# Kernel optimization log

Measured on AMD Instinct MI355X. Metric: run time of the kernel, lower is better.

The kernel has to match this reference:

```python
import jax, jax.numpy as jnp
import numpy as np

B, S, D, K = 64, 512, 512, 1024
DECAY = 0.99
EPS = 1e-05
COMMITMENT_COST = 0.25
PAD_IDX = 0


def setup_inputs() -> dict:
    key = jax.random.key(0)
    k1, k2, k3 = jax.random.split(key, 3)
    inputs = jax.random.normal(k1, (B, S, D), dtype=jnp.float32)
    padding_mask = jax.random.bernoulli(k2, 0.1, (B, S))
    codebook_w = jax.random.normal(k3, (K, D), dtype=jnp.float32) * 0.02
    codebook_w = codebook_w.at[PAD_IDX].set(0.0)  # padding_idx row zeroed
    ema_cluster_size = jnp.zeros((K,), dtype=jnp.float32)
    ema_w = codebook_w  # _ema_w initialized as copy of codebook
    return {"inputs": inputs, "padding_mask": padding_mask,
            "codebook_w": codebook_w, "ema_cluster_size": ema_cluster_size,
            "ema_w": ema_w}


def reference(inputs, padding_mask, codebook_w, ema_cluster_size, ema_w):
    input_shape = inputs.shape
    flat = inputs.reshape(-1, D)                      # [N, D]
    mask = padding_mask.reshape(-1)                   # [N], True = pad

    # squared euclidean distances: [N, K]
    dist = (jnp.sum(flat * flat, axis=1, keepdims=True)
            + jnp.sum(codebook_w * codebook_w, axis=1)
            - 2.0 * flat @ codebook_w.T)
    # non-padded tokens cannot pick code 0; padded tokens must pick code 0
    inf = jnp.float32(np.inf)
    col0 = jnp.where(mask, dist[:, 0], inf)
    rest = jnp.where(mask[:, None], inf, dist[:, 1:])
    dist = jnp.concatenate([col0[:, None], rest], axis=1)

    idx = jnp.argmin(dist, axis=1)                    # [N] int
    quantized = codebook_w[idx].reshape(input_shape)  # gather == onehot @ W

    num_nonpad = jnp.sum(~mask).astype(jnp.float32) * D
    e_latent_loss = jnp.sum((jax.lax.stop_gradient(quantized) - inputs) ** 2) / num_nonpad
    loss = COMMITMENT_COST * e_latent_loss

    # EMA codebook update (training branch, discard_ema_cluster_sizes=False)
    counts = jax.ops.segment_sum(jnp.ones_like(idx, dtype=jnp.float32), idx,
                                 num_segments=K)      # sum(encodings, 0)
    dw = jax.ops.segment_sum(flat, idx, num_segments=K)  # encodings.T @ flat
    cs = ema_cluster_size * DECAY + (1.0 - DECAY) * counts
    n = jnp.sum(cs)
    cs = (cs + EPS) / (n + K * EPS) * n
    new_ema_w = ema_w * DECAY + (1.0 - DECAY) * dw
    new_codebook = new_ema_w / cs[:, None]
    new_codebook = new_codebook.at[PAD_IDX].set(0.0)

    # straight-through estimator
    quantized_st = inputs + jax.lax.stop_gradient(quantized - inputs)

    avg_probs = counts / counts.shape[0] / (flat.shape[0] / K) if False else counts / flat.shape[0]
    perplexity = jnp.exp(-jnp.sum(avg_probs * jnp.log(avg_probs + 1e-10)))

    return (quantized_st, idx.reshape(input_shape[:-1]), loss, perplexity,
            cs, new_ema_w, new_codebook)
```

## Files before the change

### kernel.cpp

```cpp
#include <hip/hip_runtime.h>
#include <math.h>

#define N_TOK 32768
#define DDIM  512
#define KCODE 1024
#define DECAYF 0.99f
#define EPSV 1e-5f
#define CCOST 0.25f
#define MARGIN 1e-3f

typedef float f32x4 __attribute__((ext_vector_type(4)));
typedef short short8v __attribute__((ext_vector_type(8)));

__device__ __forceinline__ unsigned short f2bf(float f) {
  unsigned u = __float_as_uint(f);
  u += 0x7fffu + ((u >> 16) & 1u);
  return (unsigned short)(u >> 16);
}
__device__ __forceinline__ float bf2f(unsigned short h) {
  return __uint_as_float(((unsigned)h) << 16);
}

__device__ __forceinline__ unsigned ordf(float f) {
  unsigned u = __float_as_uint(f);
  return (u & 0x80000000u) ? ~u : (u | 0x80000000u);
}
__device__ __forceinline__ float ord2f(unsigned v) {
  unsigned u = (v & 0x80000000u) ? (v & 0x7fffffffu) : ~v;
  return __uint_as_float(u);
}
__device__ __forceinline__ void top2m(unsigned long long& a1, unsigned long long& a2,
                                      unsigned long long b1, unsigned long long b2) {
  unsigned long long m1 = a1 < b1 ? a1 : b1;
  unsigned long long hi = a1 < b1 ? b1 : a1;
  unsigned long long m2 = a2 < b2 ? a2 : b2;
  a2 = m2 < hi ? m2 : hi;
  a1 = m1;
}

__device__ __forceinline__ void stage16(const void* g, char* lds_base, int lane) {
#if __has_builtin(__builtin_amdgcn_global_load_lds)
  __builtin_amdgcn_global_load_lds((const __attribute__((address_space(1))) void*)g,
                                   (__attribute__((address_space(3))) void*)lds_base,
                                   16, 0, 0);
#else
  *(float4*)(lds_base + lane * 16) = *(const float4*)g;
#endif
}

__global__ __launch_bounds__(256) void convert_fused(
    const float* __restrict__ x, const float* __restrict__ w,
    unsigned short* __restrict__ xhi, unsigned short* __restrict__ xlo,
    unsigned short* __restrict__ whi, unsigned short* __restrict__ wlo,
    float* __restrict__ wn)
{
  int b = blockIdx.x;
  int tid = threadIdx.x;
  if (b < 16384) {
    size_t i = (size_t)b * 256 + tid;
    float4 v = *(const float4*)(x + i * 4);
    ushort4 h, l;
    h.x = f2bf(v.x); l.x = f2bf(v.x - bf2f(h.x));
    h.y = f2bf(v.y); l.y = f2bf(v.y - bf2f(h.y));
    h.z = f2bf(v.z); l.z = f2bf(v.z - bf2f(h.z));
    h.w = f2bf(v.w); l.w = f2bf(v.w - bf2f(h.w));
    *(ushort4*)(xhi + i * 4) = h;
    *(ushort4*)(xlo + i * 4) = l;
  } else {
    int k = (b - 16384) * 4 + (tid >> 6);
    int lane = tid & 63;
    double s = 0.0;
    #pragma unroll
    for (int it = 0; it < 2; it++) {
      size_t off = (size_t)k * DDIM + (lane + 64 * it) * 4;
      float4 v = *(const float4*)(w + off);
      s += (double)v.x*(double)v.x + (double)v.y*(double)v.y
         + (double)v.z*(double)v.z + (double)v.w*(double)v.w;
      ushort4 h, l;
      h.x = f2bf(v.x); l.x = f2bf(v.x - bf2f(h.x));
      h.y = f2bf(v.y); l.y = f2bf(v.y - bf2f(h.y));
      h.z = f2bf(v.z); l.z = f2bf(v.z - bf2f(h.z));
      h.w = f2bf(v.w); l.w = f2bf(v.w - bf2f(h.w));
      *(ushort4*)(whi + off) = h;
      *(ushort4*)(wlo + off) = l;
    }
    for (int o = 32; o > 0; o >>= 1) s += __shfl_down(s, o, 64);
    if (lane == 0) wn[k] = (float)s;
  }
}

__global__ __launch_bounds__(256) void dist_mfma(
    const unsigned short* __restrict__ xhi, const unsigned short* __restrict__ xlo,
    const unsigned short* __restrict__ whi, const unsigned short* __restrict__ wlo,
    const float* __restrict__ wn,
    unsigned long long* __restrict__ k1buf, unsigned long long* __restrict__ k2buf)
{
  __shared__ __align__(16) short sAh[128 * 32];
  __shared__ __align__(16) short sAl[128 * 32];
  __shared__ __align__(16) short sBh[128 * 32];
  __shared__ __align__(16) short sBl[128 * 32];
  const int tid = threadIdx.x;
  const int wv = tid >> 6, lane = tid & 63;
  const int wg = (blockIdx.x & 7) * 256 + (blockIdx.x >> 3);
  const int tb = wg >> 3, kb = wg & 7;
  const int row0 = tb * 128, col0 = kb * 128;
  const int rw = wv & 1, cw = wv >> 1;
  const int q = lane >> 4, cl = lane & 15;
  const int swz = (cl >> 1) & 3;

  f32x4 acc[4][4];
  #pragma unroll
  for (int mt = 0; mt < 4; mt++)
    #pragma unroll
    for (int nt = 0; nt < 4; nt++) acc[mt][nt] = (f32x4){0.f, 0.f, 0.f, 0.f};

  const int cA0 = wv * 64 + lane;
  const int r0 = cA0 >> 2;
  const int s0 = (cA0 & 3) ^ ((r0 >> 1) & 3);
  const size_t aoff0 = (size_t)(row0 + r0) * 1024 + (size_t)s0 * 16;
  const size_t boff0 = (size_t)(col0 + r0) * 1024 + (size_t)s0 * 16;
  const char* pxh = (const char*)xhi;
  const char* pxl = (const char*)xlo;
  const char* pwh = (const char*)whi;
  const char* pwl = (const char*)wlo;

  const int aidx = (rw * 64 + cl) * 32 + (q ^ swz) * 8;
  const int bidx = (cw * 64 + cl) * 32 + (q ^ swz) * 8;

  for (int ks = 0; ks < 16; ks++) {
    const int k2 = ks * 64;
    __syncthreads();
    stage16(pxh + aoff0 + k2,         (char*)sAh + wv * 1024, lane);
    stage16(pxh + aoff0 + 65536 + k2, (char*)sAh + (wv + 4) * 1024, lane);
    stage16(pxl + aoff0 + k2,         (char*)sAl + wv * 1024, lane);
    stage16(pxl + aoff0 + 65536 + k2, (char*)sAl + (wv + 4) * 1024, lane);
    stage16(pwh + boff0 + k2,         (char*)sBh + wv * 1024, lane);
    stage16(pwh + boff0 + 65536 + k2, (char*)sBh + (wv + 4) * 1024, lane);
    stage16(pwl + boff0 + k2,         (char*)sBl + wv * 1024, lane);
    stage16(pwl + boff0 + 65536 + k2, (char*)sBl + (wv + 4) * 1024, lane);
    __syncthreads();

    short8v ah[4], bh[4];
    #pragma unroll
    for (int mt = 0; mt < 4; mt++) ah[mt] = *(const short8v*)(sAh + aidx + mt * 512);
    #pragma unroll
    for (int nt = 0; nt < 4; nt++) bh[nt] = *(const short8v*)(sBh + bidx + nt * 512);
    #pragma unroll
    for (int mt = 0; mt < 4; mt++)
      #pragma unroll
      for (int nt = 0; nt < 4; nt++)
        acc[mt][nt] = __builtin_amdgcn_mfma_f32_16x16x32_bf16(ah[mt], bh[nt], acc[mt][nt], 0, 0, 0);

    short8v bl[4];
    #pragma unroll
    for (int nt = 0; nt < 4; nt++) bl[nt] = *(const short8v*)(sBl + bidx + nt * 512);
    #pragma unroll
    for (int mt = 0; mt < 4; mt++)
      #pragma unroll
      for (int nt = 0; nt < 4; nt++)
        acc[mt][nt] = __builtin_amdgcn_mfma_f32_16x16x32_bf16(ah[mt], bl[nt], acc[mt][nt], 0, 0, 0);

    short8v al[4];
    #pragma unroll
    for (int mt = 0; mt < 4; mt++) al[mt] = *(const short8v*)(sAl + aidx + mt * 512);
    #pragma unroll
    for (int mt = 0; mt < 4; mt++)
      #pragma unroll
      for (int nt = 0; nt < 4; nt++)
        acc[mt][nt] = __builtin_amdgcn_mfma_f32_16x16x32_bf16(al[mt], bh[nt], acc[mt][nt], 0, 0, 0);
  }

  float wnv[4];
  #pragma unroll
  for (int nt = 0; nt < 4; nt++) wnv[nt] = wn[col0 + cw * 64 + nt * 16 + cl];

  const int strip = kb * 2 + cw;
  #pragma unroll
  for (int mt = 0; mt < 4; mt++) {
    #pragma unroll
    for (int r = 0; r < 4; r++) {
      unsigned long long k1 = ~0ull, k2 = ~0ull;
      #pragma unroll
      for (int nt = 0; nt < 4; nt++) {
        int kk = col0 + cw * 64 + nt * 16 + cl;
        float dist = fmaf(-2.f, acc[mt][nt][r], wnv[nt]);
        unsigned long long key = (kk == 0) ? ~0ull
            : ((unsigned long long)ordf(dist) << 32) | (unsigned)kk;
        if (key < k1) { k2 = k1; k1 = key; }
        else if (key < k2) k2 = key;
      }
      #pragma unroll
      for (int off = 8; off > 0; off >>= 1) {
        unsigned long long o1 = __shfl_down(k1, off, 16);
        unsigned long long o2 = __shfl_down(k2, off, 16);
        top2m(k1, k2, o1, o2);
      }
      if (cl == 0) {
        int rowg = row0 + rw * 64 + mt * 16 + q * 4 + r;
        k1buf[strip * N_TOK + rowg] = k1;
        k2buf[strip * N_TOK + rowg] = k2;
      }
    }
  }
}

__global__ __launch_bounds__(1024) void combine_kernel(
    const unsigned long long* __restrict__ k1buf, const unsigned long long* __restrict__ k2buf,
    const int* __restrict__ mask,
    int* __restrict__ idx_i, int* __restrict__ flagList, int* __restrict__ flagcnt,
    int* __restrict__ counts_i)
{
  __shared__ int lh[KCODE];
  int tid = threadIdx.x;
  lh[tid] = 0;
  __syncthreads();
  int t = blockIdx.x * 1024 + tid;
  unsigned long long a1 = ~0ull, a2 = ~0ull;
  #pragma unroll
  for (int s = 0; s < 16; s++)
    top2m(a1, a2, k1buf[s * N_TOK + t], k2buf[s * N_TOK + t]);
  int bi = (int)(a1 & 0xffffffffu);
  float d1 = ord2f((unsigned)(a1 >> 32));
  float d2 = ord2f((unsigned)(a2 >> 32));
  int pad = mask[t];
  int id = pad ? 0 : bi;
  idx_i[t] = id;
  atomicAdd(&lh[id], 1);
  if (!pad && (d2 - d1) < MARGIN) {
    int p = atomicAdd(flagcnt, 1);
    flagList[p] = t;
  }
  __syncthreads();
  if (lh[tid] > 0) atomicAdd(&counts_i[tid], lh[tid]);
}

__global__ __launch_bounds__(256) void refine_kernel(
    const float* __restrict__ x, const float* __restrict__ w,
    const float* __restrict__ wn32,
    const int* __restrict__ flagList, const int* __restrict__ flagcnt,
    int* __restrict__ idx_i, int* __restrict__ counts_i)
{
  __shared__ double xd[DDIM];
  __shared__ double redbuf[4];
  __shared__ float A32sh;
  __shared__ float bv_s[256];
  __shared__ int   bi_s[256];
  int tid = threadIdx.x;
  int lane = tid & 63, wid = tid >> 6;
  int nf = *flagcnt;
  for (int fi = blockIdx.x; fi < nf; fi += gridDim.x) {
    int token = flagList[fi];
    double part = 0.0;
    for (int e = tid; e < DDIM; e += 256) {
      double v = (double)x[(size_t)token * DDIM + e];
      xd[e] = v;
      part += v * v;
    }
    for (int o = 32; o > 0; o >>= 1) part += __shfl_down(part, o, 64);
    if (lane == 0) redbuf[wid] = part;
    __syncthreads();
    if (tid == 0) {
      double a64 = redbuf[0] + redbuf[1] + redbuf[2] + redbuf[3];
      A32sh = (float)a64;
    }
    __syncthreads();
    float A32 = A32sh;
    float bv = 3.4e38f; int bi = 0x7fffffff;
    for (int k = tid; k < KCODE; k += 256) {
      if (k == 0) continue;
      const float4* wr = (const float4*)(w + (size_t)k * DDIM);
      double dot = 0.0;
      #pragma unroll 4
      for (int dq = 0; dq < DDIM / 4; dq++) {
        float4 wv = wr[dq];
        dot += xd[dq*4+0]*(double)wv.x + xd[dq*4+1]*(double)wv.y
             + xd[dq*4+2]*(double)wv.z + xd[dq*4+3]*(double)wv.w;
      }
      float M = (float)dot;
      float AB = A32 + wn32[k];
      float dist = AB - 2.0f * M;
      if (dist < bv) { bv = dist; bi = k; }
    }
    bv_s[tid] = bv; bi_s[tid] = bi;
    __syncthreads();
    for (int st = 128; st > 0; st >>= 1) {
      if (tid < st) {
        if (bv_s[tid+st] < bv_s[tid] ||
            (bv_s[tid+st] == bv_s[tid] && bi_s[tid+st] < bi_s[tid])) {
          bv_s[tid] = bv_s[tid+st]; bi_s[tid] = bi_s[tid+st];
        }
      }
      __syncthreads();
    }
    if (tid == 0) {
      int old = idx_i[token];
      int nw = bi_s[0];
      if (nw != old) {
        idx_i[token] = nw;
        atomicSub(&counts_i[old], 1);
        atomicAdd(&counts_i[nw], 1);
      }
    }
    __syncthreads();
  }
}

__global__ __launch_bounds__(1024) void scan_kernel(
    const int* __restrict__ counts_i, int* __restrict__ offsets, int* __restrict__ cursor)
{
  __shared__ int tmp[1024];
  int t = threadIdx.x;
  int c = counts_i[t];
  tmp[t] = c;
  __syncthreads();
  for (int off = 1; off < 1024; off <<= 1) {
    int v = (t >= off) ? tmp[t - off] : 0;
    __syncthreads();
    tmp[t] += v;
    __syncthreads();
  }
  int ex = tmp[t] - c;
  offsets[t] = ex;
  cursor[t] = ex;
}

__global__ __launch_bounds__(1024) void scatter_kernel(
    const int* __restrict__ idx_i, int* __restrict__ cursor, int* __restrict__ bucket)
{
  __shared__ int lh[KCODE];
  __shared__ int lb[KCODE];
  int tid = threadIdx.x;
  lh[tid] = 0;
  __syncthreads();
  int token = blockIdx.x * 1024 + tid;
  int id = idx_i[token];
  int r = atomicAdd(&lh[id], 1);
  __syncthreads();
  if (lh[tid] > 0) lb[tid] = atomicAdd(&cursor[tid], lh[tid]);
  __syncthreads();
  bucket[lb[id] + r] = token;
}

__global__ __launch_bounds__(256) void quant_kernel(
    const float* __restrict__ x, const float* __restrict__ w,
    const int* __restrict__ idx_i,
    float* __restrict__ out_q, float* __restrict__ out_idx, float* __restrict__ losssum)
{
  __shared__ float sred[4];
  int tid = threadIdx.x;
  int qd = tid & 127, h = tid >> 7;
  float s = 0.f;
  #pragma unroll
  for (int i = 0; i < 8; i++) {
    int token = blockIdx.x * 16 + i * 2 + h;
    int idx = idx_i[token];
    float4 xv = *(const float4*)(x + (size_t)token * DDIM + qd * 4);
    float4 wv = *(const float4*)(w + (size_t)idx * DDIM + qd * 4);
    *(float4*)(out_q + (size_t)token * DDIM + qd * 4) = wv;
    if (qd == 0) out_idx[token] = (float)idx;
    float dx = wv.x - xv.x, dy = wv.y - xv.y, dz = wv.z - xv.z, dww = wv.w - xv.w;
    s += dx*dx + dy*dy + dz*dz + dww*dww;
  }
  for (int o = 32; o > 0; o >>= 1) s += __shfl_down(s, o, 64);
  int lane = tid & 63, wid = tid >> 6;
  if (lane == 0) sred[wid] = s;
  __syncthreads();
  if (tid == 0) atomicAdd(losssum, sred[0] + sred[1] + sred[2] + sred[3]);
}

__global__ __launch_bounds__(128) void dw_kernel(
    const float* __restrict__ x, const int* __restrict__ bucket,
    const int* __restrict__ idx_i, float* __restrict__ dw)
{
  int b0 = blockIdx.x * 32;
  int t = threadIdx.x;
  int ent = bucket[b0 + (t & 31)];
  int eid = idx_i[ent];
  int tok0 = __shfl(ent, 0, 64);
  int cur  = __shfl(eid, 0, 64);
  float4 acc = make_float4(0.f, 0.f, 0.f, 0.f);
  float4 nv = *(const float4*)(x + (size_t)tok0 * DDIM + t * 4);
  for (int j = 0; j < 32; j++) {
    float4 v = nv;
    int id = __shfl(eid, j, 64);
    if (j < 31) {
      int tn = __shfl(ent, j + 1, 64);
      nv = *(const float4*)(x + (size_t)tn * DDIM + t * 4);
    }
    if (id != cur) {
      float* p = dw + (size_t)cur * DDIM + t * 4;
      atomicAdd(p + 0, acc.x); atomicAdd(p + 1, acc.y);
      atomicAdd(p + 2, acc.z); atomicAdd(p + 3, acc.w);
      acc = make_float4(0.f, 0.f, 0.f, 0.f);
      cur = id;
    }
    acc.x += v.x; acc.y += v.y; acc.z += v.z; acc.w += v.w;
  }
  float* p = dw + (size_t)cur * DDIM + t * 4;
  atomicAdd(p + 0, acc.x); atomicAdd(p + 1, acc.y);
  atomicAdd(p + 2, acc.z); atomicAdd(p + 3, acc.w);
}

__global__ __launch_bounds__(1024) void stats_kernel(
    const int* __restrict__ counts_i, const float* __restrict__ ema_cs,
    const float* __restrict__ losssum,
    float* __restrict__ out_loss, float* __restrict__ out_perp,
    float* __restrict__ out_cs)
{
  __shared__ float sbuf[17];
  int k = threadIdx.x;
  float cnt = (float)counts_i[k];
  float csr = ema_cs[k] * DECAYF + (1.f - DECAYF) * cnt;
  float v = csr;
  for (int o = 32; o > 0; o >>= 1) v += __shfl_down(v, o, 64);
  int lane = k & 63, wid = k >> 6;
  if (lane == 0) sbuf[wid] = v;
  __syncthreads();
  if (k == 0) { float n = 0.f; for (int i = 0; i < 16; i++) n += sbuf[i]; sbuf[16] = n; }
  __syncthreads();
  float n = sbuf[16];
  out_cs[k] = (csr + EPSV) / (n + (float)KCODE * EPSV) * n;
  __syncthreads();
  float p = cnt / (float)N_TOK;
  v = p * logf(p + 1e-10f);
  for (int o = 32; o > 0; o >>= 1) v += __shfl_down(v, o, 64);
  if (lane == 0) sbuf[wid] = v;
  __syncthreads();
  if (k == 0) {
    float s = 0.f; for (int i = 0; i < 16; i++) s += sbuf[i];
    out_perp[0] = expf(-s);
    float nonpad = (float)(N_TOK - counts_i[0]);
    out_loss[0] = CCOST * losssum[0] / (nonpad * (float)DDIM);
  }
}

__global__ __launch_bounds__(256) void ema_kernel(
    const float* __restrict__ ema_w, const float* __restrict__ dw,
    const float* __restrict__ cs,
    float* __restrict__ out_ema, float* __restrict__ out_cb)
{
  int i = blockIdx.x * 256 + threadIdx.x;
  int e = i * 4;
  int k = e >> 9;
  float4 dv = *(const float4*)(dw + e);
  float4 ew = *(const float4*)(ema_w + e);
  float4 ne;
  ne.x = ew.x * DECAYF + (1.f - DECAYF) * dv.x;
  ne.y = ew.y * DECAYF + (1.f - DECAYF) * dv.y;
  ne.z = ew.z * DECAYF + (1.f - DECAYF) * dv.z;
  ne.w = ew.w * DECAYF + (1.f - DECAYF) * dv.w;
  *(float4*)(out_ema + e) = ne;
  float4 cb;
  if (k == 0) { cb.x = 0.f; cb.y = 0.f; cb.z = 0.f; cb.w = 0.f; }
  else {
    float csk = cs[k];
    cb.x = ne.x / csk; cb.y = ne.y / csk; cb.z = ne.z / csk; cb.w = ne.w / csk;
  }
  *(float4*)(out_cb + e) = cb;
}

extern "C" void kernel_launch(void* const* d_in, const int* in_sizes, int n_in,
                              void* d_out, int out_size, void* d_ws, size_t ws_size,
                              hipStream_t stream) {
  const float* x      = (const float*)d_in[0];
  const int*   mask   = (const int*)d_in[1];
  const float* w      = (const float*)d_in[2];
  const float* ema_cs = (const float*)d_in[3];
  const float* ema_w  = (const float*)d_in[4];
  float* out = (float*)d_out;

  float* out_q    = out;
  float* out_idx  = out + 16777216;
  float* out_loss = out + 16809984;
  float* out_perp = out + 16809985;
  float* out_cs   = out + 16809986;
  float* out_ema  = out + 16811010;
  float* out_cb   = out + 17335298;

  unsigned short* xhi = (unsigned short*)out_q;
  unsigned short* xlo = xhi + (size_t)N_TOK * DDIM;

  char* ws = (char*)d_ws;
  int*   counts_i = (int*)  (ws + 0);
  float* dw       = (float*)(ws + 4096);
  float* losssum  = (float*)(ws + 2101248);
  int*   flagcnt  = (int*)  (ws + 2101252);
  int*   offsets  = (int*)  (ws + 2101312);
  int*   cursor   = (int*)  (ws + 2105408);
  float* wn       = (float*)(ws + 2109504);
  int*   idx_i    = (int*)  (ws + 2113600);
  int*   bucket   = (int*)  (ws + 2244672);
  unsigned short* whi = (unsigned short*)(ws + 2375744);
  unsigned short* wlo = (unsigned short*)(ws + 3424320);
  unsigned long long* k1buf = (unsigned long long*)(ws + 4472896);
  unsigned long long* k2buf = (unsigned long long*)(ws + 8667200);
  int*   flagList = (int*)  (ws + 12861504);

  hipMemsetAsync(ws, 0, 2101256, stream);
  convert_fused<<<16384 + 256, 256, 0, stream>>>(x, w, xhi, xlo, whi, wlo, wn);
  dist_mfma<<<(N_TOK / 128) * 8, 256, 0, stream>>>(xhi, xlo, whi, wlo, wn, k1buf, k2buf);
  combine_kernel<<<N_TOK / 1024, 1024, 0, stream>>>(k1buf, k2buf, mask, idx_i, flagList, flagcnt, counts_i);
  refine_kernel<<<1024, 256, 0, stream>>>(x, w, wn, flagList, flagcnt, idx_i, counts_i);
  scan_kernel<<<1, 1024, 0, stream>>>(counts_i, offsets, cursor);
  scatter_kernel<<<N_TOK / 1024, 1024, 0, stream>>>(idx_i, cursor, bucket);
  quant_kernel<<<N_TOK / 16, 256, 0, stream>>>(x, w, idx_i, out_q, out_idx, losssum);
  dw_kernel<<<N_TOK / 32, 128, 0, stream>>>(x, bucket, idx_i, dw);
  stats_kernel<<<1, 1024, 0, stream>>>(counts_i, ema_cs, losssum, out_loss, out_perp, out_cs);
  ema_kernel<<<KCODE * DDIM / 4 / 256, 256, 0, stream>>>(ema_w, dw, out_cs, out_ema, out_cb);
}
```

Before: 409.4 us.

## Double-buffer LDS tiles in distance GEMM and raise MFMA wave priority

The distance MFMA kernel now keeps two sets of LDS buffers, so global-to-LDS staging of the next K-slice is issued before the MFMAs on the current slice run. This removes one barrier per step and lets memory loads overlap with compute. s_setprio is also raised around the MFMA bursts to favour math issue. The cost is doubled LDS use (64KB per block), which may lower occupancy.

```diff
diff --git a/kernel.cpp b/kernel.cpp
--- a/kernel.cpp
+++ b/kernel.cpp
@@ -95,10 +95,14 @@
     const float* __restrict__ wn,
     unsigned long long* __restrict__ k1buf, unsigned long long* __restrict__ k2buf)
 {
-  __shared__ __align__(16) short sAh[128 * 32];
-  __shared__ __align__(16) short sAl[128 * 32];
-  __shared__ __align__(16) short sBh[128 * 32];
-  __shared__ __align__(16) short sBl[128 * 32];
+  __shared__ __align__(16) short sAh0[128 * 32];
+  __shared__ __align__(16) short sAl0[128 * 32];
+  __shared__ __align__(16) short sBh0[128 * 32];
+  __shared__ __align__(16) short sBl0[128 * 32];
+  __shared__ __align__(16) short sAh1[128 * 32];
+  __shared__ __align__(16) short sAl1[128 * 32];
+  __shared__ __align__(16) short sBh1[128 * 32];
+  __shared__ __align__(16) short sBl1[128 * 32];
   const int tid = threadIdx.x;
   const int wv = tid >> 6, lane = tid & 63;
   const int wg = (blockIdx.x & 7) * 256 + (blockIdx.x >> 3);
@@ -127,48 +131,67 @@
   const int aidx = (rw * 64 + cl) * 32 + (q ^ swz) * 8;
   const int bidx = (cw * 64 + cl) * 32 + (q ^ swz) * 8;
 
-  for (int ks = 0; ks < 16; ks++) {
-    const int k2 = ks * 64;
-    __syncthreads();
-    stage16(pxh + aoff0 + k2,         (char*)sAh + wv * 1024, lane);
-    stage16(pxh + aoff0 + 65536 + k2, (char*)sAh + (wv + 4) * 1024, lane);
-    stage16(pxl + aoff0 + k2,         (char*)sAl + wv * 1024, lane);
-    stage16(pxl + aoff0 + 65536 + k2, (char*)sAl + (wv + 4) * 1024, lane);
-    stage16(pwh + boff0 + k2,         (char*)sBh + wv * 1024, lane);
-    stage16(pwh + boff0 + 65536 + k2, (char*)sBh + (wv + 4) * 1024, lane);
-    stage16(pwl + boff0 + k2,         (char*)sBl + wv * 1024, lane);
-    stage16(pwl + boff0 + 65536 + k2, (char*)sBl + (wv + 4) * 1024, lane);
-    __syncthreads();
-
-    short8v ah[4], bh[4];
-    #pragma unroll
-    for (int mt = 0; mt < 4; mt++) ah[mt] = *(const short8v*)(sAh + aidx + mt * 512);
-    #pragma unroll
-    for (int nt = 0; nt < 4; nt++) bh[nt] = *(const short8v*)(sBh + bidx + nt * 512);
-    #pragma unroll
-    for (int mt = 0; mt < 4; mt++)
-      #pragma unroll
-      for (int nt = 0; nt < 4; nt++)
-        acc[mt][nt] = __builtin_amdgcn_mfma_f32_16x16x32_bf16(ah[mt], bh[nt], acc[mt][nt], 0, 0, 0);
-
-    short8v bl[4];
-    #pragma unroll
-    for (int nt = 0; nt < 4; nt++) bl[nt] = *(const short8v*)(sBl + bidx + nt * 512);
-    #pragma unroll
-    for (int mt = 0; mt < 4; mt++)
-      #pragma unroll
-      for (int nt = 0; nt < 4; nt++)
-        acc[mt][nt] = __builtin_amdgcn_mfma_f32_16x16x32_bf16(ah[mt], bl[nt], acc[mt][nt], 0, 0, 0);
-
-    short8v al[4];
-    #pragma unroll
-    for (int mt = 0; mt < 4; mt++) al[mt] = *(const short8v*)(sAl + aidx + mt * 512);
-    #pragma unroll
-    for (int mt = 0; mt < 4; mt++)
-      #pragma unroll
-      for (int nt = 0; nt < 4; nt++)
-        acc[mt][nt] = __builtin_amdgcn_mfma_f32_16x16x32_bf16(al[mt], bh[nt], acc[mt][nt], 0, 0, 0);
-  }
+#define STAGE_STEP(KS, AH, AL, BH, BL) do {                                   \
+    const int kk2_ = (KS) * 64;                                               \
+    stage16(pxh + aoff0 + kk2_,         (char*)(AH) + wv * 1024, lane);       \
+    stage16(pxh + aoff0 + 65536 + kk2_, (char*)(AH) + (wv + 4) * 1024, lane); \
+    stage16(pxl + aoff0 + kk2_,         (char*)(AL) + wv * 1024, lane);       \
+    stage16(pxl + aoff0 + 65536 + kk2_, (char*)(AL) + (wv + 4) * 1024, lane); \
+    stage16(pwh + boff0 + kk2_,         (char*)(BH) + wv * 1024, lane);       \
+    stage16(pwh + boff0 + 65536 + kk2_, (char*)(BH) + (wv + 4) * 1024, lane); \
+    stage16(pwl + boff0 + kk2_,         (char*)(BL) + wv * 1024, lane);       \
+    stage16(pwl + boff0 + 65536 + kk2_, (char*)(BL) + (wv + 4) * 1024, lane); \
+  } while (0)
+
+#define COMPUTE_STEP(AH, AL, BH, BL) do {                                     \
+    short8v ah_[4], bh_[4];                                                   \
+    _Pragma("unroll")                                                         \
+    for (int mt = 0; mt < 4; mt++) ah_[mt] = *(const short8v*)((AH) + aidx + mt * 512); \
+    _Pragma("unroll")                                                         \
+    for (int nt = 0; nt < 4; nt++) bh_[nt] = *(const short8v*)((BH) + bidx + nt * 512); \
+    __builtin_amdgcn_s_setprio(1);                                            \
+    _Pragma("unroll")                                                         \
+    for (int mt = 0; mt < 4; mt++)                                            \
+      _Pragma("unroll")                                                       \
+      for (int nt = 0; nt < 4; nt++)                                          \
+        acc[mt][nt] = __builtin_amdgcn_mfma_f32_16x16x32_bf16(ah_[mt], bh_[nt], acc[mt][nt], 0, 0, 0); \
+    __builtin_amdgcn_s_setprio(0);                                            \
+    short8v bl_[4];                                                           \
+    _Pragma("unroll")                                                         \
+    for (int nt = 0; nt < 4; nt++) bl_[nt] = *(const short8v*)((BL) + bidx + nt * 512); \
+    __builtin_amdgcn_s_setprio(1);                                            \
+    _Pragma("unroll")                                                         \
+    for (int mt = 0; mt < 4; mt++)                                            \
+      _Pragma("unroll")                                                       \
+      for (int nt = 0; nt < 4; nt++)                                          \
+        acc[mt][nt] = __builtin_amdgcn_mfma_f32_16x16x32_bf16(ah_[mt], bl_[nt], acc[mt][nt], 0, 0, 0); \
+    __builtin_amdgcn_s_setprio(0);                                            \
+    short8v al_[4];                                                           \
+    _Pragma("unroll")                                                         \
+    for (int mt = 0; mt < 4; mt++) al_[mt] = *(const short8v*)((AL) + aidx + mt * 512); \
+    __builtin_amdgcn_s_setprio(1);                                            \
+    _Pragma("unroll")                                                         \
+    for (int mt = 0; mt < 4; mt++)                                            \
+      _Pragma("unroll")                                                       \
+      for (int nt = 0; nt < 4; nt++)                                          \
+        acc[mt][nt] = __builtin_amdgcn_mfma_f32_16x16x32_bf16(al_[mt], bh_[nt], acc[mt][nt], 0, 0, 0); \
+    __builtin_amdgcn_s_setprio(0);                                            \
+  } while (0)
+
+  STAGE_STEP(0, sAh0, sAl0, sBh0, sBl0);
+  __syncthreads();
+
+  #pragma unroll 1
+  for (int ks = 0; ks < 16; ks += 2) {
+    STAGE_STEP(ks + 1, sAh1, sAl1, sBh1, sBl1);
+    COMPUTE_STEP(sAh0, sAl0, sBh0, sBl0);
+    __syncthreads();
+    if (ks + 2 < 16) STAGE_STEP(ks + 2, sAh0, sAl0, sBh0, sBl0);
+    COMPUTE_STEP(sAh1, sAl1, sBh1, sBl1);
+    __syncthreads();
+  }
+#undef STAGE_STEP
+#undef COMPUTE_STEP
 
   float wnv[4];
   #pragma unroll
```

Result: no change. 403.1 us (-1.6%).

## Drop split-bf16 low parts; use single bf16 GEMM with wider refine margin

Applied to the files above, without the earlier changes.

Stops computing bf16 low-residual halves of inputs and codebook, and the distance GEMM now runs one bf16 MFMA pass per tile instead of three (hi*hi, hi*lo, lo*hi). This cuts conversion traffic, LDS staging and MFMA work to about a third. To make up for the lower precision, the top-2 ambiguity margin goes from 1e-3 to 0.05, so more tokens get flagged for exact fp32 refinement, and the refine kernel grid is doubled to handle them. The risk is a much larger refine workload and possible wrong argmin picks if the margin is too tight for plain bf16 error.

```diff
diff --git a/kernel.cpp b/kernel.cpp
--- a/kernel.cpp
+++ b/kernel.cpp
@@ -7,7 +7,7 @@
 #define DECAYF 0.99f
 #define EPSV 1e-5f
 #define CCOST 0.25f
-#define MARGIN 1e-3f
+#define MARGIN 0.05f
 
 typedef float f32x4 __attribute__((ext_vector_type(4)));
 typedef short short8v __attribute__((ext_vector_type(8)));
@@ -50,8 +50,7 @@
 
 __global__ __launch_bounds__(256) void convert_fused(
     const float* __restrict__ x, const float* __restrict__ w,
-    unsigned short* __restrict__ xhi, unsigned short* __restrict__ xlo,
-    unsigned short* __restrict__ whi, unsigned short* __restrict__ wlo,
+    unsigned short* __restrict__ xhi, unsigned short* __restrict__ whi,
     float* __restrict__ wn)
 {
   int b = blockIdx.x;
@@ -59,13 +58,12 @@
   if (b < 16384) {
     size_t i = (size_t)b * 256 + tid;
     float4 v = *(const float4*)(x + i * 4);
-    ushort4 h, l;
-    h.x = f2bf(v.x); l.x = f2bf(v.x - bf2f(h.x));
-    h.y = f2bf(v.y); l.y = f2bf(v.y - bf2f(h.y));
-    h.z = f2bf(v.z); l.z = f2bf(v.z - bf2f(h.z));
-    h.w = f2bf(v.w); l.w = f2bf(v.w - bf2f(h.w));
+    ushort4 h;
+    h.x = f2bf(v.x);
+    h.y = f2bf(v.y);
+    h.z = f2bf(v.z);
+    h.w = f2bf(v.w);
     *(ushort4*)(xhi + i * 4) = h;
-    *(ushort4*)(xlo + i * 4) = l;
   } else {
     int k = (b - 16384) * 4 + (tid >> 6);
     int lane = tid & 63;
@@ -76,13 +74,12 @@
       float4 v = *(const float4*)(w + off);
       s += (double)v.x*(double)v.x + (double)v.y*(double)v.y
          + (double)v.z*(double)v.z + (double)v.w*(double)v.w;
-      ushort4 h, l;
-      h.x = f2bf(v.x); l.x = f2bf(v.x - bf2f(h.x));
-      h.y = f2bf(v.y); l.y = f2bf(v.y - bf2f(h.y));
-      h.z = f2bf(v.z); l.z = f2bf(v.z - bf2f(h.z));
-      h.w = f2bf(v.w); l.w = f2bf(v.w - bf2f(h.w));
+      ushort4 h;
+      h.x = f2bf(v.x);
+      h.y = f2bf(v.y);
+      h.z = f2bf(v.z);
+      h.w = f2bf(v.w);
       *(ushort4*)(whi + off) = h;
-      *(ushort4*)(wlo + off) = l;
     }
     for (int o = 32; o > 0; o >>= 1) s += __shfl_down(s, o, 64);
     if (lane == 0) wn[k] = (float)s;
@@ -90,15 +87,12 @@
 }
 
 __global__ __launch_bounds__(256) void dist_mfma(
-    const unsigned short* __restrict__ xhi, const unsigned short* __restrict__ xlo,
-    const unsigned short* __restrict__ whi, const unsigned short* __restrict__ wlo,
+    const unsigned short* __restrict__ xhi, const unsigned short* __restrict__ whi,
     const float* __restrict__ wn,
     unsigned long long* __restrict__ k1buf, unsigned long long* __restrict__ k2buf)
 {
-  __shared__ __align__(16) short sAh[128 * 32];
-  __shared__ __align__(16) short sAl[128 * 32];
-  __shared__ __align__(16) short sBh[128 * 32];
-  __shared__ __align__(16) short sBl[128 * 32];
+  __shared__ __align__(16) short sA[128 * 32];
+  __shared__ __align__(16) short sB[128 * 32];
   const int tid = threadIdx.x;
   const int wv = tid >> 6, lane = tid & 63;
   const int wg = (blockIdx.x & 7) * 256 + (blockIdx.x >> 3);
@@ -120,9 +114,7 @@
   const size_t aoff0 = (size_t)(row0 + r0) * 1024 + (size_t)s0 * 16;
   const size_t boff0 = (size_t)(col0 + r0) * 1024 + (size_t)s0 * 16;
   const char* pxh = (const char*)xhi;
-  const char* pxl = (const char*)xlo;
   const char* pwh = (const char*)whi;
-  const char* pwl = (const char*)wlo;
 
   const int aidx = (rw * 64 + cl) * 32 + (q ^ swz) * 8;
   const int bidx = (cw * 64 + cl) * 32 + (q ^ swz) * 8;
@@ -130,44 +122,22 @@
   for (int ks = 0; ks < 16; ks++) {
     const int k2 = ks * 64;
     __syncthreads();
-    stage16(pxh + aoff0 + k2,         (char*)sAh + wv * 1024, lane);
-    stage16(pxh + aoff0 + 65536 + k2, (char*)sAh + (wv + 4) * 1024, lane);
-    stage16(pxl + aoff0 + k2,         (char*)sAl + wv * 1024, lane);
-    stage16(pxl + aoff0 + 65536 + k2, (char*)sAl + (wv + 4) * 1024, lane);
-    stage16(pwh + boff0 + k2,         (char*)sBh + wv * 1024, lane);
-    stage16(pwh + boff0 + 65536 + k2, (char*)sBh + (wv + 4) * 1024, lane);
-    stage16(pwl + boff0 + k2,         (char*)sBl + wv * 1024, lane);
-    stage16(pwl + boff0 + 65536 + k2, (char*)sBl + (wv + 4) * 1024, lane);
-    __syncthreads();
-
-    short8v ah[4], bh[4];
-    #pragma unroll
-    for (int mt = 0; mt < 4; mt++) ah[mt] = *(const short8v*)(sAh + aidx + mt * 512);
-    #pragma unroll
-    for (int nt = 0; nt < 4; nt++) bh[nt] = *(const short8v*)(sBh + bidx + nt * 512);
+    stage16(pxh + aoff0 + k2,         (char*)sA + wv * 1024, lane);
+    stage16(pxh + aoff0 + 65536 + k2, (char*)sA + (wv + 4) * 1024, lane);
+    stage16(pwh + boff0 + k2,         (char*)sB + wv * 1024, lane);
+    stage16(pwh + boff0 + 65536 + k2, (char*)sB + (wv + 4) * 1024, lane);
+    __syncthreads();
+
+    short8v a[4], b[4];
+    #pragma unroll
+    for (int mt = 0; mt < 4; mt++) a[mt] = *(const short8v*)(sA + aidx + mt * 512);
+    #pragma unroll
+    for (int nt = 0; nt < 4; nt++) b[nt] = *(const short8v*)(sB + bidx + nt * 512);
     #pragma unroll
     for (int mt = 0; mt < 4; mt++)
       #pragma unroll
       for (int nt = 0; nt < 4; nt++)
-        acc[mt][nt] = __builtin_amdgcn_mfma_f32_16x16x32_bf16(ah[mt], bh[nt], acc[mt][nt], 0, 0, 0);
-
-    short8v bl[4];
-    #pragma unroll
-    for (int nt = 0; nt < 4; nt++) bl[nt] = *(const short8v*)(sBl + bidx + nt * 512);
-    #pragma unroll
-    for (int mt = 0; mt < 4; mt++)
-      #pragma unroll
-      for (int nt = 0; nt < 4; nt++)
-        acc[mt][nt] = __builtin_amdgcn_mfma_f32_16x16x32_bf16(ah[mt], bl[nt], acc[mt][nt], 0, 0, 0);
-
-    short8v al[4];
-    #pragma unroll
-    for (int mt = 0; mt < 4; mt++) al[mt] = *(const short8v*)(sAl + aidx + mt * 512);
-    #pragma unroll
-    for (int mt = 0; mt < 4; mt++)
-      #pragma unroll
-      for (int nt = 0; nt < 4; nt++)
-        acc[mt][nt] = __builtin_amdgcn_mfma_f32_16x16x32_bf16(al[mt], bh[nt], acc[mt][nt], 0, 0, 0);
+        acc[mt][nt] = __builtin_amdgcn_mfma_f32_16x16x32_bf16(a[mt], b[nt], acc[mt][nt], 0, 0, 0);
   }
 
   float wnv[4];
@@ -478,7 +448,6 @@
   float* out_cb   = out + 17335298;
 
   unsigned short* xhi = (unsigned short*)out_q;
-  unsigned short* xlo = xhi + (size_t)N_TOK * DDIM;
 
   char* ws = (char*)d_ws;
   int*   counts_i = (int*)  (ws + 0);
@@ -491,16 +460,15 @@
   int*   idx_i    = (int*)  (ws + 2113600);
   int*   bucket   = (int*)  (ws + 2244672);
   unsigned short* whi = (unsigned short*)(ws + 2375744);
-  unsigned short* wlo = (unsigned short*)(ws + 3424320);
   unsigned long long* k1buf = (unsigned long long*)(ws + 4472896);
   unsigned long long* k2buf = (unsigned long long*)(ws + 8667200);
   int*   flagList = (int*)  (ws + 12861504);
 
   hipMemsetAsync(ws, 0, 2101256, stream);
-  convert_fused<<<16384 + 256, 256, 0, stream>>>(x, w, xhi, xlo, whi, wlo, wn);
-  dist_mfma<<<(N_TOK / 128) * 8, 256, 0, stream>>>(xhi, xlo, whi, wlo, wn, k1buf, k2buf);
+  convert_fused<<<16384 + 256, 256, 0, stream>>>(x, w, xhi, whi, wn);
+  dist_mfma<<<(N_TOK / 128) * 8, 256, 0, stream>>>(xhi, whi, wn, k1buf, k2buf);
   combine_kernel<<<N_TOK / 1024, 1024, 0, stream>>>(k1buf, k2buf, mask, idx_i, flagList, flagcnt, counts_i);
-  refine_kernel<<<1024, 256, 0, stream>>>(x, w, wn, flagList, flagcnt, idx_i, counts_i);
+  refine_kernel<<<2048, 256, 0, stream>>>(x, w, wn, flagList, flagcnt, idx_i, counts_i);
   scan_kernel<<<1, 1024, 0, stream>>>(counts_i, offsets, cursor);
   scatter_kernel<<<N_TOK / 1024, 1024, 0, stream>>>(idx_i, cursor, bucket);
   quant_kernel<<<N_TOK / 16, 256, 0, stream>>>(x, w, idx_i, out_q, out_idx, losssum);
```

Result: slower. 1.429 ms (+249.0%).
